# Performance work log

Hardware: AMD Instinct MI355X
Metric: run time of the kernel (lower is better)

Reference implementation:

```python
import jax, jax.numpy as jnp
import numpy as np
import math

WIDTH = 1024
NUM_HEADS = 16
HEAD_DIM = WIDTH // NUM_HEADS
WINDOW_SIZE = 256
MIN_LOGITS_VALUE = -1e30


def setup_inputs() -> dict:
    key = jax.random.key(0)
    ks = jax.random.split(key, 7)
    b, t = 2, 2048
    std = math.sqrt(1.0 / WIDTH)
    x = jax.random.normal(ks[0], (b, t, WIDTH), dtype=jnp.float32)
    segment_pos = jnp.broadcast_to(jnp.arange(t, dtype=jnp.int32)[None, :], (b, t))
    Wq = jax.random.normal(ks[1], (WIDTH, WIDTH), dtype=jnp.float32) * std
    Wk = jax.random.normal(ks[2], (HEAD_DIM, WIDTH), dtype=jnp.float32) * std
    Wv = jax.random.normal(ks[3], (HEAD_DIM, WIDTH), dtype=jnp.float32) * std
    Wf = jax.random.normal(ks[4], (WIDTH, WIDTH), dtype=jnp.float32) * std
    bf = jnp.zeros((WIDTH,), dtype=jnp.float32)
    return {"x": x, "segment_pos": segment_pos, "Wq": Wq, "Wk": Wk, "Wv": Wv, "Wf": Wf, "bf": bf}


def reference(x, segment_pos, Wq, Wk, Wv, Wf, bf):
    b, t, _ = x.shape
    # projections (Linear: x @ W.T)
    q = (x @ Wq.T).reshape(b, t, NUM_HEADS, HEAD_DIM)  # [b,t,n,h]
    k = x @ Wk.T  # [b,t,h] single shared KV head (MQA)
    v = x @ Wv.T  # [b,t,h]
    scale = 1.0 / math.sqrt(HEAD_DIM)
    logits = jnp.einsum('btnh,bsh->bnts', q, k) * scale  # [b,n,t,s]
    # sliding-window causal mask: q_pos >= k_pos and q_pos <= k_pos + window
    ar = jnp.arange(t)
    qp = ar[:, None]
    kp = ar[None, :]
    mask = (qp >= kp) & (qp <= kp + WINDOW_SIZE)  # [t,s]
    masked = jnp.where(mask[None, None, :, :], logits, MIN_LOGITS_VALUE)
    probs = jax.nn.softmax(masked.astype(jnp.float32), axis=-1).astype(logits.dtype)
    out = jnp.einsum('bnts,bsh->btnh', probs, v)  # [b,t,n,h]
    out = out.reshape(b, t, WIDTH)
    return out @ Wf.T + bf
```

## Files before the change

### kernel.cpp

```cpp
#include <hip/hip_runtime.h>
#include <stdint.h>

#define B_SZ   2
#define T_SEQ  2048
#define WIDTH_ 1024
#define NH     16
#define HD     64
#define WIN    256
#define MROWS  (B_SZ * T_SEQ)
#define NQKV   1152

typedef __attribute__((ext_vector_type(4))) float f32x4;
typedef __attribute__((ext_vector_type(8))) short s16x8;

typedef __attribute__((address_space(1))) const void gas_void;
typedef __attribute__((address_space(3))) void las_void;

#define MFMA(a, b, c) __builtin_amdgcn_mfma_f32_16x16x32_bf16((a), (b), (c), 0, 0, 0)

#define VM_WAIT4() asm volatile("s_waitcnt vmcnt(4)" ::: "memory")
#define VM_WAIT0() asm volatile("s_waitcnt vmcnt(0)" ::: "memory")

__device__ __forceinline__ void gload_lds16(const void* g, void* l) {
  __builtin_amdgcn_global_load_lds((gas_void*)g, (las_void*)l, 16, 0, 0);
}

__device__ __forceinline__ ushort f2bf(float f) {
  union { float f; uint32_t u; } v; v.f = f;
  uint32_t u = v.u;
  return (ushort)((u + 0x7FFFu + ((u >> 16) & 1u)) >> 16);
}

__global__ void prep_kernel(const float* __restrict__ x,
                            const float* __restrict__ Wq,
                            const float* __restrict__ Wk,
                            const float* __restrict__ Wv,
                            const float* __restrict__ Wf,
                            ushort* __restrict__ xb,
                            ushort* __restrict__ wqkv,
                            ushort* __restrict__ wfb) {
  const int XN = MROWS * WIDTH_ / 4;
  const int WQ = NQKV * WIDTH_ / 4;
  const int WF = WIDTH_ * WIDTH_ / 4;
  int i = blockIdx.x * blockDim.x + threadIdx.x;
  float4 v;
  ushort* dst;
  if (i < XN) {
    v = ((const float4*)x)[i];
    dst = xb + i * 4;
  } else if (i < XN + WQ) {
    int j = i - XN;
    int row = (j * 4) >> 10;
    int col = (j * 4) & 1023;
    const float* src = (row < 1024) ? (Wq + row * 1024 + col)
                     : (row < 1088) ? (Wk + (row - 1024) * 1024 + col)
                                    : (Wv + (row - 1088) * 1024 + col);
    v = *(const float4*)src;
    dst = wqkv + j * 4;
  } else if (i < XN + WQ + WF) {
    int j = i - XN - WQ;
    v = ((const float4*)Wf)[j];
    dst = wfb + j * 4;
  } else {
    return;
  }
  ushort4 o;
  o.x = f2bf(v.x); o.y = f2bf(v.y); o.z = f2bf(v.z); o.w = f2bf(v.w);
  *(ushort4*)dst = o;
}

#define G_STAGE64(AS, BS, KOFF) do {                                        \
  _Pragma("unroll")                                                         \
  for (int i_ = 0; i_ < 2; ++i_) {                                          \
    int c_ = i_ * 256 + w * 64 + lane;                          \
    int row_ = c_ >> 3;                         \
    int ke_ = ((c_ & 7) * 8) ^ ((row_ & 7) << 3);      \
    int ldsb_ = (i_ * 256 + w * 64) * 16;            \
    gload_lds16(A + (size_t)(m0 + row_) * 1024 + (KOFF) + ke_,              \
                (char*)(AS) + ldsb_);                                       \
    gload_lds16(B + (size_t)(n0 + row_) * 1024 + (KOFF) + ke_,              \
                (char*)(BS) + ldsb_);                                       \
  }                                                                         \
} while (0)

#define G_COMPUTE64(AS, BS) do {                                            \
  _Pragma("unroll")                                                         \
  for (int ks_ = 0; ks_ < 2; ++ks_) {                                       \
    s16x8 af_[2], bf_[2];                                                   \
    _Pragma("unroll")                                                       \
    for (int t_ = 0; t_ < 2; ++t_) {                                        \
      int ra_ = wm + t_ * 16 + r16;                                         \
      int rb_ = wn + t_ * 16 + r16;                                         \
      af_[t_] = *(const s16x8*)&(AS)[ra_ * 64 +                             \
                  ((ks_ * 32 + g * 8) ^ ((ra_ & 7) << 3))];                 \
      bf_[t_] = *(const s16x8*)&(BS)[rb_ * 64 +                             \
                  ((ks_ * 32 + g * 8) ^ ((rb_ & 7) << 3))];                 \
    }                                                                       \
    _Pragma("unroll")                                                       \
    for (int mb_ = 0; mb_ < 2; ++mb_)                                       \
      _Pragma("unroll")                                                     \
      for (int nb_ = 0; nb_ < 2; ++nb_)                                     \
        acc[mb_][nb_] = MFMA(af_[mb_], bf_[nb_], acc[mb_][nb_]);            \
  }                                                                         \
} while (0)

#define G_ITER(AS, BS, K)  do {                                             \
  if ((K) == 960) { VM_WAIT0(); } else { VM_WAIT4(); }                      \
  __syncthreads();                                                          \
  G_COMPUTE64(AS, BS);                                                      \
  __syncthreads();                                                          \
  if ((K) + 128 < 1024) G_STAGE64(AS, BS, (K) + 128);                       \
} while (0)

template <int MODE>
__global__ __launch_bounds__(256) void gemm_kernel(
    const ushort* __restrict__ A, const ushort* __restrict__ B,
    ushort* __restrict__ qb, ushort* __restrict__ kb, ushort* __restrict__ vt,
    float* __restrict__ Cf, const float* __restrict__ bias) {
  const int NBX = (MODE == 0) ? 18 : 16;
  const int nwg = NBX * 64;
  const int cpx = nwg >> 3;
  int swz = (blockIdx.x & 7) * cpx + (blockIdx.x >> 3);
  const int bx = swz % NBX;
  const int by = swz / NBX;

  const int w = threadIdx.x >> 6;
  const int lane = threadIdx.x & 63;
  const int g = lane >> 4;
  const int r16 = lane & 15;
  const int m0 = by * 64;
  const int n0 = bx * 64;
  const int wm = (w >> 1) * 32;
  const int wn = (w & 1) * 32;

  __shared__ ushort As0[64 * 64];
  __shared__ ushort Bs0[64 * 64];
  __shared__ ushort As1[64 * 64];
  __shared__ ushort Bs1[64 * 64];

  f32x4 acc[2][2] = {};

  G_STAGE64(As0, Bs0, 0);
  G_STAGE64(As1, Bs1, 64);
#pragma unroll
  for (int k0 = 0; k0 < 1024; k0 += 128) {
    G_ITER(As0, Bs0, k0);
    G_ITER(As1, Bs1, k0 + 64);
  }

#pragma unroll
  for (int mb = 0; mb < 2; ++mb)
#pragma unroll
    for (int nb = 0; nb < 2; ++nb) {
      int n = n0 + wn + nb * 16 + r16;
      int mbase = m0 + wm + mb * 16 + 4 * g;
      if (MODE == 0) {
#pragma unroll
        for (int r = 0; r < 4; ++r) {
          ushort h = f2bf(acc[mb][nb][r]);
          int m = mbase + r;
          if (n < 1024)      qb[m * 1024 + n] = h;
          else if (n < 1088) kb[m * 64 + (n - 1024)] = h;
          else               vt[((size_t)((m >> 11) * 64 + (n - 1088))) * 2048 +
                                (m & 2047)] = h;
        }
      } else {
        float bv = bias[n];
#pragma unroll
        for (int r = 0; r < 4; ++r)
          Cf[(size_t)(mbase + r) * 1024 + n] = acc[mb][nb][r] + bv;
      }
    }
}

__global__ __launch_bounds__(64, 2) void attn_kernel(
    const ushort* __restrict__ qb, const ushort* __restrict__ kb,
    const ushort* __restrict__ vt, ushort* __restrict__ ao) {
  const int lane = threadIdx.x;
  const int g = lane >> 4;
  const int r16 = lane & 15;
  const int blk = blockIdx.x;
  const int qt = blk & 63;
  const int h = (blk >> 6) & 15;
  const int b = blk >> 10;
  const int q0 = qt * 32;
  const int qpA = q0 + r16;
  const int qpB = q0 + 16 + r16;

  const ushort* qrowA = qb + (size_t)(b * 2048 + qpA) * 1024 + h * 64;
  const ushort* qrowB = qb + (size_t)(b * 2048 + qpB) * 1024 + h * 64;
  s16x8 qfA0 = *(const s16x8*)(qrowA + g * 8);
  s16x8 qfA1 = *(const s16x8*)(qrowA + 32 + g * 8);
  s16x8 qfB0 = *(const s16x8*)(qrowB + g * 8);
  s16x8 qfB1 = *(const s16x8*)(qrowB + 32 + g * 8);

  f32x4 oaccA[4] = {}, oaccB[4] = {};
  float mA = -1e30f, lA = 0.f, mB = -1e30f, lB = 0.f;

  int kt0 = q0 - WIN;
  if (kt0 < 0) kt0 = 0;
  kt0 &= ~31;

  s16x8 pk[4][2];
#pragma unroll
  for (int s = 0; s < 4; ++s) {
    const ushort* kp = kb + (size_t)(b * 2048 + kt0 + s * 16 + r16) * 64;
    pk[s][0] = *(const s16x8*)(kp + g * 8);
    pk[s][1] = *(const s16x8*)(kp + 32 + g * 8);
  }

  for (int kt = kt0; kt <= q0; kt += 64) {
    s16x8 c[4][2];
#pragma unroll
    for (int s = 0; s < 4; ++s) { c[s][0] = pk[s][0]; c[s][1] = pk[s][1]; }

    s16x8 vfr[4][2];
#pragma unroll
    for (int db = 0; db < 4; ++db) {
      const ushort* vrow = vt + (size_t)(b * 64 + db * 16 + r16) * 2048 + kt;
      uint2 va0 = *(const uint2*)(vrow + 4 * g);
      uint2 va1 = *(const uint2*)(vrow + 16 + 4 * g);
      uint2 vb0 = *(const uint2*)(vrow + 32 + 4 * g);
      uint2 vb1 = *(const uint2*)(vrow + 48 + 4 * g);
      union { s16x8 v; uint32_t d[4]; } u0, u1;
      u0.d[0] = va0.x; u0.d[1] = va0.y; u0.d[2] = va1.x; u0.d[3] = va1.y;
      u1.d[0] = vb0.x; u1.d[1] = vb0.y; u1.d[2] = vb1.x; u1.d[3] = vb1.y;
      vfr[db][0] = u0.v; vfr[db][1] = u1.v;
    }

    if (kt + 64 <= q0) {
#pragma unroll
      for (int s = 0; s < 4; ++s) {
        const ushort* kp = kb + (size_t)(b * 2048 + kt + 64 + s * 16 + r16) * 64;
        pk[s][0] = *(const s16x8*)(kp + g * 8);
        pk[s][1] = *(const s16x8*)(kp + 32 + g * 8);
      }
    }

    f32x4 sA[4], sB[4];
    __builtin_amdgcn_s_setprio(1);
#pragma unroll
    for (int s = 0; s < 4; ++s) {
      f32x4 z = {};
      sA[s] = MFMA(c[s][0], qfA0, z); sA[s] = MFMA(c[s][1], qfA1, sA[s]);
      sB[s] = MFMA(c[s][0], qfB0, z); sB[s] = MFMA(c[s][1], qfB1, sB[s]);
    }
    __builtin_amdgcn_s_setprio(0);

    float pA[4][4], pB[4][4];
    float tmA = -1e30f, tmB = -1e30f;
#pragma unroll
    for (int s = 0; s < 4; ++s)
#pragma unroll
      for (int r = 0; r < 4; ++r) {
        int ka = kt + s * 16 + 4 * g + r;
        float a = (ka <= qpA && qpA - ka <= WIN) ? sA[s][r] * 0.125f : -1e30f;
        float bv = (ka <= qpB && qpB - ka <= WIN) ? sB[s][r] * 0.125f : -1e30f;
        pA[s][r] = a; pB[s][r] = bv;
        tmA = fmaxf(tmA, a); tmB = fmaxf(tmB, bv);
      }
    tmA = fmaxf(tmA, __shfl_xor(tmA, 16));
    tmA = fmaxf(tmA, __shfl_xor(tmA, 32));
    tmB = fmaxf(tmB, __shfl_xor(tmB, 16));
    tmB = fmaxf(tmB, __shfl_xor(tmB, 32));

    float mnA = fmaxf(mA, tmA), mnB = fmaxf(mB, tmB);
    float corrA = __expf(mA - mnA), corrB = __expf(mB - mnB);
    float tsA = 0.f, tsB = 0.f;
    s16x8 pfA0, pfA1, pfB0, pfB1;
#pragma unroll
    for (int r = 0; r < 4; ++r) {
      float eA0 = __expf(pA[0][r] - mnA);
      float eA1 = __expf(pA[1][r] - mnA);
      float eA2 = __expf(pA[2][r] - mnA);
      float eA3 = __expf(pA[3][r] - mnA);
      float eB0 = __expf(pB[0][r] - mnB);
      float eB1 = __expf(pB[1][r] - mnB);
      float eB2 = __expf(pB[2][r] - mnB);
      float eB3 = __expf(pB[3][r] - mnB);
      tsA += (eA0 + eA1) + (eA2 + eA3);
      tsB += (eB0 + eB1) + (eB2 + eB3);
      pfA0[r] = (short)f2bf(eA0); pfA0[4 + r] = (short)f2bf(eA1);
      pfA1[r] = (short)f2bf(eA2); pfA1[4 + r] = (short)f2bf(eA3);
      pfB0[r] = (short)f2bf(eB0); pfB0[4 + r] = (short)f2bf(eB1);
      pfB1[r] = (short)f2bf(eB2); pfB1[4 + r] = (short)f2bf(eB3);
    }
    tsA += __shfl_xor(tsA, 16); tsA += __shfl_xor(tsA, 32);
    tsB += __shfl_xor(tsB, 16); tsB += __shfl_xor(tsB, 32);
    lA = lA * corrA + tsA; mA = mnA;
    lB = lB * corrB + tsB; mB = mnB;

#pragma unroll
    for (int db = 0; db < 4; ++db) { oaccA[db] *= corrA; oaccB[db] *= corrB; }

    __builtin_amdgcn_s_setprio(1);
#pragma unroll
    for (int db = 0; db < 4; ++db) {
      oaccA[db] = MFMA(vfr[db][0], pfA0, oaccA[db]);
      oaccA[db] = MFMA(vfr[db][1], pfA1, oaccA[db]);
      oaccB[db] = MFMA(vfr[db][0], pfB0, oaccB[db]);
      oaccB[db] = MFMA(vfr[db][1], pfB1, oaccB[db]);
    }
    __builtin_amdgcn_s_setprio(0);
  }

  float invA = 1.0f / lA, invB = 1.0f / lB;
  ushort* orowA = ao + (size_t)(b * 2048 + qpA) * 1024 + h * 64;
  ushort* orowB = ao + (size_t)(b * 2048 + qpB) * 1024 + h * 64;
#pragma unroll
  for (int db = 0; db < 4; ++db) {
    ushort4 oA, oB;
    oA.x = f2bf(oaccA[db][0] * invA); oA.y = f2bf(oaccA[db][1] * invA);
    oA.z = f2bf(oaccA[db][2] * invA); oA.w = f2bf(oaccA[db][3] * invA);
    oB.x = f2bf(oaccB[db][0] * invB); oB.y = f2bf(oaccB[db][1] * invB);
    oB.z = f2bf(oaccB[db][2] * invB); oB.w = f2bf(oaccB[db][3] * invB);
    *(ushort4*)(orowA + db * 16 + 4 * g) = oA;
    *(ushort4*)(orowB + db * 16 + 4 * g) = oB;
  }
}

extern "C" void kernel_launch(void* const* d_in, const int* in_sizes, int n_in,
                              void* d_out, int out_size, void* d_ws, size_t ws_size,
                              hipStream_t stream) {
  const float* x  = (const float*)d_in[0];
  const float* Wq = (const float*)d_in[2];
  const float* Wk = (const float*)d_in[3];
  const float* Wv = (const float*)d_in[4];
  const float* Wf = (const float*)d_in[5];
  const float* bf = (const float*)d_in[6];
  float* out = (float*)d_out;

  uint8_t* w8 = (uint8_t*)d_ws;
  ushort* xb   = (ushort*)(w8 + 0);
  ushort* qbuf = (ushort*)(w8 + 8388608);
  ushort* attn = (ushort*)(w8 + 16777216);
  ushort* wqkv = (ushort*)(w8 + 25165824);
  ushort* wfb  = (ushort*)(w8 + 27525120);
  ushort* kbuf = (ushort*)(w8 + 29622272);
  ushort* vt   = (ushort*)(w8 + 30146560);

  prep_kernel<<<6272, 256, 0, stream>>>(x, Wq, Wk, Wv, Wf, xb, wqkv, wfb);
  gemm_kernel<0><<<1152, 256, 0, stream>>>(xb, wqkv, qbuf, kbuf, vt,
                                           nullptr, nullptr);
  attn_kernel<<<2048, 64, 0, stream>>>(qbuf, kbuf, vt, attn);
  gemm_kernel<1><<<1024, 256, 0, stream>>>(attn, wfb, nullptr, nullptr,
                                           nullptr, out, bf);
}
```

Measured before the change: 152.9 us.

## Fuse fp32-to-bf16 conversion into GEMM loads and enlarge tiles to 128x64

Removes the separate prep kernel and has both GEMMs read fp32 x and weights directly, converting to bf16 in registers before writing to padded LDS. The GEMM tile grows from 64x64 to 128x64 with 2x4 MFMA blocks per wave, halving the grid. Register-staged prefetch replaces the async global_load_lds double buffering. This saves one launch and the bf16 round trip through memory, but weights are re-read as fp32 and converted by every block, which doubles their load traffic and adds conversion ALU work.

```diff
diff --git a/kernel.cpp b/kernel.cpp
--- a/kernel.cpp
+++ b/kernel.cpp
@@ -8,22 +8,11 @@
 #define HD     64
 #define WIN    256
 #define MROWS  (B_SZ * T_SEQ)
-#define NQKV   1152
 
 typedef __attribute__((ext_vector_type(4))) float f32x4;
 typedef __attribute__((ext_vector_type(8))) short s16x8;
 
-typedef __attribute__((address_space(1))) const void gas_void;
-typedef __attribute__((address_space(3))) void las_void;
-
 #define MFMA(a, b, c) __builtin_amdgcn_mfma_f32_16x16x32_bf16((a), (b), (c), 0, 0, 0)
-
-#define VM_WAIT4() asm volatile("s_waitcnt vmcnt(4)" ::: "memory")
-#define VM_WAIT0() asm volatile("s_waitcnt vmcnt(0)" ::: "memory")
-
-__device__ __forceinline__ void gload_lds16(const void* g, void* l) {
-  __builtin_amdgcn_global_load_lds((gas_void*)g, (las_void*)l, 16, 0, 0);
-}
 
 __device__ __forceinline__ ushort f2bf(float f) {
   union { float f; uint32_t u; } v; v.f = f;
@@ -31,138 +20,160 @@
   return (ushort)((u + 0x7FFFu + ((u >> 16) & 1u)) >> 16);
 }
 
-__global__ void prep_kernel(const float* __restrict__ x,
-                            const float* __restrict__ Wq,
-                            const float* __restrict__ Wk,
-                            const float* __restrict__ Wv,
-                            const float* __restrict__ Wf,
-                            ushort* __restrict__ xb,
-                            ushort* __restrict__ wqkv,
-                            ushort* __restrict__ wfb) {
-  const int XN = MROWS * WIDTH_ / 4;
-  const int WQ = NQKV * WIDTH_ / 4;
-  const int WF = WIDTH_ * WIDTH_ / 4;
-  int i = blockIdx.x * blockDim.x + threadIdx.x;
-  float4 v;
-  ushort* dst;
-  if (i < XN) {
-    v = ((const float4*)x)[i];
-    dst = xb + i * 4;
-  } else if (i < XN + WQ) {
-    int j = i - XN;
-    int row = (j * 4) >> 10;
-    int col = (j * 4) & 1023;
-    const float* src = (row < 1024) ? (Wq + row * 1024 + col)
-                     : (row < 1088) ? (Wk + (row - 1024) * 1024 + col)
-                                    : (Wv + (row - 1088) * 1024 + col);
-    v = *(const float4*)src;
-    dst = wqkv + j * 4;
-  } else if (i < XN + WQ + WF) {
-    int j = i - XN - WQ;
-    v = ((const float4*)Wf)[j];
-    dst = wfb + j * 4;
-  } else {
-    return;
-  }
-  ushort4 o;
-  o.x = f2bf(v.x); o.y = f2bf(v.y); o.z = f2bf(v.z); o.w = f2bf(v.w);
-  *(ushort4*)dst = o;
-}
-
-#define G_STAGE64(AS, BS, KOFF) do {                                        \
-  _Pragma("unroll")                                                         \
-  for (int i_ = 0; i_ < 2; ++i_) {                                          \
-    int c_ = i_ * 256 + w * 64 + lane;                          \
-    int row_ = c_ >> 3;                         \
-    int ke_ = ((c_ & 7) * 8) ^ ((row_ & 7) << 3);      \
-    int ldsb_ = (i_ * 256 + w * 64) * 16;            \
-    gload_lds16(A + (size_t)(m0 + row_) * 1024 + (KOFF) + ke_,              \
-                (char*)(AS) + ldsb_);                                       \
-    gload_lds16(B + (size_t)(n0 + row_) * 1024 + (KOFF) + ke_,              \
-                (char*)(BS) + ldsb_);                                       \
-  }                                                                         \
-} while (0)
-
-#define G_COMPUTE64(AS, BS) do {                                            \
-  _Pragma("unroll")                                                         \
-  for (int ks_ = 0; ks_ < 2; ++ks_) {                                       \
-    s16x8 af_[2], bf_[2];                                                   \
-    _Pragma("unroll")                                                       \
-    for (int t_ = 0; t_ < 2; ++t_) {                                        \
-      int ra_ = wm + t_ * 16 + r16;                                         \
-      int rb_ = wn + t_ * 16 + r16;                                         \
-      af_[t_] = *(const s16x8*)&(AS)[ra_ * 64 +                             \
-                  ((ks_ * 32 + g * 8) ^ ((ra_ & 7) << 3))];                 \
-      bf_[t_] = *(const s16x8*)&(BS)[rb_ * 64 +                             \
-                  ((ks_ * 32 + g * 8) ^ ((rb_ & 7) << 3))];                 \
-    }                                                                       \
-    _Pragma("unroll")                                                       \
-    for (int mb_ = 0; mb_ < 2; ++mb_)                                       \
-      _Pragma("unroll")                                                     \
-      for (int nb_ = 0; nb_ < 2; ++nb_)                                     \
-        acc[mb_][nb_] = MFMA(af_[mb_], bf_[nb_], acc[mb_][nb_]);            \
-  }                                                                         \
-} while (0)
-
-#define G_ITER(AS, BS, K)  do {                                             \
-  if ((K) == 960) { VM_WAIT0(); } else { VM_WAIT4(); }                      \
-  __syncthreads();                                                          \
-  G_COMPUTE64(AS, BS);                                                      \
-  __syncthreads();                                                          \
-  if ((K) + 128 < 1024) G_STAGE64(AS, BS, (K) + 128);                       \
-} while (0)
-
 template <int MODE>
-__global__ __launch_bounds__(256) void gemm_kernel(
-    const ushort* __restrict__ A, const ushort* __restrict__ B,
+__global__ __launch_bounds__(256, 3) void gemm_kernel(
+    const void* __restrict__ A0, const float* __restrict__ B0,
+    const float* __restrict__ B1, const float* __restrict__ B2,
     ushort* __restrict__ qb, ushort* __restrict__ kb, ushort* __restrict__ vt,
     float* __restrict__ Cf, const float* __restrict__ bias) {
   const int NBX = (MODE == 0) ? 18 : 16;
-  const int nwg = NBX * 64;
+  const int nwg = NBX * 32;
   const int cpx = nwg >> 3;
-  int swz = (blockIdx.x & 7) * cpx + (blockIdx.x >> 3);
+  int swz = ((int)blockIdx.x & 7) * cpx + ((int)blockIdx.x >> 3);
   const int bx = swz % NBX;
   const int by = swz / NBX;
 
-  const int w = threadIdx.x >> 6;
-  const int lane = threadIdx.x & 63;
+  const int tid = threadIdx.x;
+  const int w = tid >> 6;
+  const int lane = tid & 63;
   const int g = lane >> 4;
   const int r16 = lane & 15;
-  const int m0 = by * 64;
+  const int m0 = by * 128;
   const int n0 = bx * 64;
-  const int wm = (w >> 1) * 32;
-  const int wn = (w & 1) * 32;
-
-  __shared__ ushort As0[64 * 64];
-  __shared__ ushort Bs0[64 * 64];
-  __shared__ ushort As1[64 * 64];
-  __shared__ ushort Bs1[64 * 64];
-
-  f32x4 acc[2][2] = {};
-
-  G_STAGE64(As0, Bs0, 0);
-  G_STAGE64(As1, Bs1, 64);
-#pragma unroll
-  for (int k0 = 0; k0 < 1024; k0 += 128) {
-    G_ITER(As0, Bs0, k0);
-    G_ITER(As1, Bs1, k0 + 64);
+  const int wm = w * 32;
+
+  const float* Brow;
+  if (MODE == 0)
+    Brow = (bx < 16) ? B0 + (size_t)n0 * 1024 : (bx == 16 ? B1 : B2);
+  else
+    Brow = B0 + (size_t)n0 * 1024;
+
+  __shared__ ushort As[128 * 72];
+  __shared__ ushort Bs[64 * 72];
+
+  f32x4 acc[2][4] = {};
+
+  f32x4 aRf[8];
+  s16x8 aRh[4];
+  f32x4 bR[4];
+
+#define LOAD_A(K) do {                                                      \
+  if (MODE == 0) {                                                          \
+    const float* xp = (const float*)A0;                                     \
+    _Pragma("unroll")                                                       \
+    for (int i_ = 0; i_ < 8; ++i_) {                                        \
+      int q_ = tid + i_ * 256;                                 \
+      int rt_ = q_ >> 4, c4_ = q_ & 15;                                     \
+      aRf[i_] = *(const f32x4*)(xp + (size_t)(m0 + rt_) * 1024 + (K) +      \
+                                c4_ * 4);                                   \
+    }                                                                       \
+  } else {                                                                  \
+    const ushort* ap = (const ushort*)A0;                                   \
+    _Pragma("unroll")                                                       \
+    for (int i_ = 0; i_ < 4; ++i_) {                                        \
+      int q_ = tid + i_ * 256;                                 \
+      int rt_ = q_ >> 3, c8_ = q_ & 7;                                      \
+      aRh[i_] = *(const s16x8*)(ap + (size_t)(m0 + rt_) * 1024 + (K) +      \
+                                c8_ * 8);                                   \
+    }                                                                       \
+  }                                                                         \
+} while (0)
+
+#define LOAD_B(K) do {                                                      \
+  _Pragma("unroll")                                                         \
+  for (int i_ = 0; i_ < 4; ++i_) {                                          \
+    int q_ = tid + i_ * 256;                                   \
+    int rt_ = q_ >> 4, c4_ = q_ & 15;                                       \
+    bR[i_] = *(const f32x4*)(Brow + (size_t)rt_ * 1024 + (K) + c4_ * 4);    \
+  }                                                                         \
+} while (0)
+
+#define STORE_AB() do {                                                     \
+  if (MODE == 0) {                                                          \
+    _Pragma("unroll")                                                       \
+    for (int i_ = 0; i_ < 8; ++i_) {                                        \
+      int q_ = tid + i_ * 256;                                              \
+      int rt_ = q_ >> 4, c4_ = q_ & 15;                                     \
+      ushort4 o_;                                                           \
+      o_.x = f2bf(aRf[i_][0]); o_.y = f2bf(aRf[i_][1]);                     \
+      o_.z = f2bf(aRf[i_][2]); o_.w = f2bf(aRf[i_][3]);                     \
+      *(ushort4*)&As[rt_ * 72 + c4_ * 4] = o_;                              \
+    }                                                                       \
+  } else {                                                                  \
+    _Pragma("unroll")                                                       \
+    for (int i_ = 0; i_ < 4; ++i_) {                                        \
+      int q_ = tid + i_ * 256;                                              \
+      int rt_ = q_ >> 3, c8_ = q_ & 7;                                      \
+      *(s16x8*)&As[rt_ * 72 + c8_ * 8] = aRh[i_];                           \
+    }                                                                       \
+  }                                                                         \
+  _Pragma("unroll")                                                         \
+  for (int i_ = 0; i_ < 4; ++i_) {                                          \
+    int q_ = tid + i_ * 256;                                                \
+    int rt_ = q_ >> 4, c4_ = q_ & 15;                                       \
+    ushort4 o_;                                                             \
+    o_.x = f2bf(bR[i_][0]); o_.y = f2bf(bR[i_][1]);                         \
+    o_.z = f2bf(bR[i_][2]); o_.w = f2bf(bR[i_][3]);                         \
+    *(ushort4*)&Bs[rt_ * 72 + c4_ * 4] = o_;                                \
+  }                                                                         \
+} while (0)
+
+#define COMPUTE() do {                                                      \
+  _Pragma("unroll")                                                         \
+  for (int ks_ = 0; ks_ < 2; ++ks_) {                                       \
+    s16x8 af_[2], bf_[4];                                                   \
+    _Pragma("unroll")                                                       \
+    for (int mb_ = 0; mb_ < 2; ++mb_)                                       \
+      af_[mb_] = *(const s16x8*)&As[(wm + mb_ * 16 + r16) * 72 +            \
+                                    ks_ * 32 + g * 8];                      \
+    _Pragma("unroll")                                                       \
+    for (int nb_ = 0; nb_ < 4; ++nb_)                                       \
+      bf_[nb_] = *(const s16x8*)&Bs[(nb_ * 16 + r16) * 72 +                 \
+                                    ks_ * 32 + g * 8];                      \
+    _Pragma("unroll")                                                       \
+    for (int mb_ = 0; mb_ < 2; ++mb_)                                       \
+      _Pragma("unroll")                                                     \
+      for (int nb_ = 0; nb_ < 4; ++nb_)                                     \
+        acc[mb_][nb_] = MFMA(af_[mb_], bf_[nb_], acc[mb_][nb_]);            \
+  }                                                                         \
+} while (0)
+
+  LOAD_A(0); LOAD_B(0);
+  STORE_AB();
+  __syncthreads();
+  for (int k0 = 0; k0 < 1024; k0 += 64) {
+    const bool more = (k0 + 64 < 1024);
+    if (more) { LOAD_A(k0 + 64); LOAD_B(k0 + 64); }
+    COMPUTE();
+    __syncthreads();
+    if (more) {
+      STORE_AB();
+      __syncthreads();
+    }
   }
 
 #pragma unroll
   for (int mb = 0; mb < 2; ++mb)
 #pragma unroll
-    for (int nb = 0; nb < 2; ++nb) {
-      int n = n0 + wn + nb * 16 + r16;
+    for (int nb = 0; nb < 4; ++nb) {
+      int n = n0 + nb * 16 + r16;
       int mbase = m0 + wm + mb * 16 + 4 * g;
       if (MODE == 0) {
-#pragma unroll
-        for (int r = 0; r < 4; ++r) {
-          ushort h = f2bf(acc[mb][nb][r]);
-          int m = mbase + r;
-          if (n < 1024)      qb[m * 1024 + n] = h;
-          else if (n < 1088) kb[m * 64 + (n - 1024)] = h;
-          else               vt[((size_t)((m >> 11) * 64 + (n - 1088))) * 2048 +
-                                (m & 2047)] = h;
+        if (bx < 16) {
+#pragma unroll
+          for (int r = 0; r < 4; ++r)
+            qb[(mbase + r) * 1024 + n] = f2bf(acc[mb][nb][r]);
+        } else if (bx == 16) {
+#pragma unroll
+          for (int r = 0; r < 4; ++r)
+            kb[(mbase + r) * 64 + (n & 63)] = f2bf(acc[mb][nb][r]);
+        } else {
+#pragma unroll
+          for (int r = 0; r < 4; ++r) {
+            int m = mbase + r;
+            vt[((size_t)((m >> 11) * 64 + (n & 63))) * 2048 + (m & 2047)] =
+                f2bf(acc[mb][nb][r]);
+          }
         }
       } else {
         float bv = bias[n];
@@ -171,6 +182,10 @@
           Cf[(size_t)(mbase + r) * 1024 + n] = acc[mb][nb][r] + bv;
       }
     }
+#undef LOAD_A
+#undef LOAD_B
+#undef STORE_AB
+#undef COMPUTE
 }
 
 __global__ __launch_bounds__(64, 2) void attn_kernel(
@@ -331,18 +346,14 @@
   float* out = (float*)d_out;
 
   uint8_t* w8 = (uint8_t*)d_ws;
-  ushort* xb   = (ushort*)(w8 + 0);
-  ushort* qbuf = (ushort*)(w8 + 8388608);
-  ushort* attn = (ushort*)(w8 + 16777216);
-  ushort* wqkv = (ushort*)(w8 + 25165824);
-  ushort* wfb  = (ushort*)(w8 + 27525120);
-  ushort* kbuf = (ushort*)(w8 + 29622272);
-  ushort* vt   = (ushort*)(w8 + 30146560);
-
-  prep_kernel<<<6272, 256, 0, stream>>>(x, Wq, Wk, Wv, Wf, xb, wqkv, wfb);
-  gemm_kernel<0><<<1152, 256, 0, stream>>>(xb, wqkv, qbuf, kbuf, vt,
-                                           nullptr, nullptr);
+  ushort* qbuf = (ushort*)(w8 + 0);
+  ushort* attn = (ushort*)(w8 + 8388608);
+  ushort* kbuf = (ushort*)(w8 + 16777216);
+  ushort* vt   = (ushort*)(w8 + 17301504);
+
+  gemm_kernel<0><<<576, 256, 0, stream>>>(x, Wq, Wk, Wv,
+                                          qbuf, kbuf, vt, nullptr, nullptr);
   attn_kernel<<<2048, 64, 0, stream>>>(qbuf, kbuf, vt, attn);
-  gemm_kernel<1><<<1024, 256, 0, stream>>>(attn, wfb, nullptr, nullptr,
-                                           nullptr, out, bf);
+  gemm_kernel<1><<<512, 256, 0, stream>>>(attn, Wf, nullptr, nullptr,
+                                          nullptr, nullptr, nullptr, out, bf);
 }
```

After: 161.3 us. 5.5% more time.
